# Kernel optimization log

Hardware: AMD Instinct MI355X
Metric: run time of the kernel (lower is better)

## Reference

```python
import jax, jax.numpy as jnp
import numpy as np

D_MODEL = 1024
NUM_HEADS = 16
HEAD_DIM = D_MODEL // NUM_HEADS
B, S = 4, 2048


def setup_inputs() -> dict:
    key = jax.random.key(0)
    ks = jax.random.split(key, 11)
    s = 1.0 / np.sqrt(D_MODEL)
    inp = {
        "query": jax.random.normal(ks[0], (B, S, D_MODEL), jnp.float32),
        "key": jax.random.normal(ks[1], (B, S, D_MODEL), jnp.float32),
        "value": jax.random.normal(ks[2], (B, S, D_MODEL), jnp.float32),
        "Wq": jax.random.uniform(ks[3], (D_MODEL, D_MODEL), jnp.float32, -s, s),
        "bq": jax.random.uniform(ks[4], (D_MODEL,), jnp.float32, -s, s),
        "Wk": jax.random.uniform(ks[5], (D_MODEL, D_MODEL), jnp.float32, -s, s),
        "bk": jax.random.uniform(ks[6], (D_MODEL,), jnp.float32, -s, s),
        "Wv": jax.random.uniform(ks[7], (D_MODEL, D_MODEL), jnp.float32, -s, s),
        "bv": jax.random.uniform(ks[8], (D_MODEL,), jnp.float32, -s, s),
        "Wo": jax.random.uniform(ks[9], (D_MODEL, D_MODEL), jnp.float32, -s, s),
        "bo": jax.random.uniform(ks[10], (D_MODEL,), jnp.float32, -s, s),
    }
    return inp


def reference(query, key, value, Wq, bq, Wk, bk, Wv, bv, Wo, bo):
    B_, Sq, _ = query.shape
    # torch Linear: x @ W.T + b
    q = (query @ Wq.T + bq).reshape(B_, Sq, NUM_HEADS, HEAD_DIM).transpose(0, 2, 1, 3)  # [B,H,Sq,Dh]
    k = (key @ Wk.T + bk).reshape(B_, -1, NUM_HEADS, HEAD_DIM).transpose(0, 2, 1, 3)
    v = (value @ Wv.T + bv).reshape(B_, -1, NUM_HEADS, HEAD_DIM).transpose(0, 2, 1, 3)
    scores = jnp.einsum("bhqd,bhkd->bhqk", q, k) / np.sqrt(HEAD_DIM)
    attn = jax.nn.softmax(scores, axis=-1)
    x = jnp.einsum("bhqk,bhkd->bhqd", attn, v)  # [B,H,Sq,Dh]
    x = x.transpose(0, 2, 1, 3).reshape(B_, Sq, D_MODEL)
    return x @ Wo.T + bo
```

## Files before the change

kernel.cpp:

```cpp
#include <hip/hip_runtime.h>
#include <hip/hip_bf16.h>
#include <stdint.h>


typedef __attribute__((ext_vector_type(4))) float f32x4;
typedef __attribute__((ext_vector_type(16))) float f32x16;
typedef __attribute__((ext_vector_type(8))) short short8;
typedef __attribute__((ext_vector_type(4))) unsigned short ushort4v;
typedef __attribute__((ext_vector_type(4))) unsigned int uint4v;

#define SCALE_Q 0.1803368801111f
#define EXP2(x) __builtin_amdgcn_exp2f(x)

__device__ __forceinline__ unsigned short f2bf(float f) {
    union { float f; unsigned int u; } v; v.f = f;
    unsigned int u = v.u;
    u += 0x7FFFu + ((u >> 16) & 1u);
    return (unsigned short)(u >> 16);
}

__device__ __forceinline__ void gll16(const void* g, void* l) {
    __builtin_amdgcn_global_load_lds(
        (const __attribute__((address_space(1))) void*)g,
        (__attribute__((address_space(3))) void*)l, 16, 0, 0);
}

__device__ __forceinline__ unsigned int cvtpk_bf16(float lo, float hi) {
    unsigned int r;
    asm("v_cvt_pk_bf16_f32 %0, %1, %2" : "=v"(r) : "v"(lo), "v"(hi));
    return r;
}
#define PLSWAP(a, b) asm("v_permlane32_swap_b32 %0, %1" : "+v"(a), "+v"(b))

__global__ __launch_bounds__(256) void cvtW(const float* __restrict__ s0, const float* __restrict__ s1,
                                            const float* __restrict__ s2, const float* __restrict__ s3,
                                            unsigned short* __restrict__ d0, unsigned short* __restrict__ d1,
                                            unsigned short* __restrict__ d2, unsigned short* __restrict__ d3) {
    int t = blockIdx.x >> 10;
    const float* sp = (t == 0) ? s0 : (t == 1) ? s1 : (t == 2) ? s2 : s3;
    unsigned short* dp = (t == 0) ? d0 : (t == 1) ? d1 : (t == 2) ? d2 : d3;
    int j = ((blockIdx.x & 1023) * 256 + threadIdx.x) * 4;
    float4 v = *(const float4*)(sp + j);
    ushort4v o; o.x = f2bf(v.x); o.y = f2bf(v.y); o.z = f2bf(v.z); o.w = f2bf(v.w);
    *(ushort4v*)(dp + j) = o;
}

__global__ __launch_bounds__(256, 2)
void proj3(const float* __restrict__ Aq, const float* __restrict__ Ak, const float* __restrict__ Av,
           const unsigned short* __restrict__ Wq, const unsigned short* __restrict__ Wk,
           const unsigned short* __restrict__ Wv,
           const float* __restrict__ bq, const float* __restrict__ bk, const float* __restrict__ bv,
           unsigned short* __restrict__ Cq, unsigned short* __restrict__ Ck,
           unsigned short* __restrict__ Cv) {
    __shared__ unsigned short As[128 * 32];
    __shared__ unsigned short Bs[128 * 32];
    const int tid = threadIdx.x;
    const int wid = tid >> 6, lane = tid & 63;
    const int seg = blockIdx.x >> 9, idx = blockIdx.x & 511;
    const float* Af = (seg == 0) ? Aq : (seg == 1) ? Ak : Av;
    const unsigned short* Bw = (seg == 0) ? Wq : (seg == 1) ? Wk : Wv;
    const float* bias = (seg == 0) ? bq : (seg == 1) ? bk : bv;
    unsigned short* C = (seg == 0) ? Cq : (seg == 1) ? Ck : Cv;

    const int xcd = idx & 7, j_ = idx >> 3;
    const int mtile = xcd * 8 + (j_ >> 3), ntile = j_ & 7;
    const int m0 = mtile * 128, n0 = ntile * 128;
    const int wm = (wid >> 1) * 64, wn = (wid & 1) * 64;

    f32x4 acc[4][4];
#pragma unroll
    for (int i = 0; i < 4; i++)
#pragma unroll
        for (int j = 0; j < 4; j++) acc[i][j] = f32x4{0.f, 0.f, 0.f, 0.f};

    const int srow = tid >> 2, scol = (tid & 3) * 8;
    const unsigned short* gB0 = Bw + (size_t)(n0 + srow) * 1024 + scol;
    const unsigned short* gB1 = Bw + (size_t)(n0 + 64 + srow) * 1024 + scol;
    char* lB0 = (char*)Bs + wid * 1024;
    char* lB1 = (char*)Bs + 4096 + wid * 1024;
    const float* gAf0 = Af + (size_t)(m0 + srow) * 1024 + scol;
    const float* gAf1 = Af + (size_t)(m0 + 64 + srow) * 1024 + scol;

    const int frow = lane & 15;
    const int fcol = (lane >> 4) * 16;

    float4 p00 = *(const float4*)(gAf0);
    float4 p01 = *(const float4*)(gAf0 + 4);
    float4 p10 = *(const float4*)(gAf1);
    float4 p11 = *(const float4*)(gAf1 + 4);

    for (int k0 = 0; k0 < 1024; k0 += 32) {
        gll16(gB0 + k0, lB0);
        gll16(gB1 + k0, lB1);
        {
            uint4v wa = {cvtpk_bf16(p00.x, p00.y), cvtpk_bf16(p00.z, p00.w),
                         cvtpk_bf16(p01.x, p01.y), cvtpk_bf16(p01.z, p01.w)};
            uint4v wb = {cvtpk_bf16(p10.x, p10.y), cvtpk_bf16(p10.z, p10.w),
                         cvtpk_bf16(p11.x, p11.y), cvtpk_bf16(p11.z, p11.w)};
            *(uint4v*)((char*)As + tid * 16) = wa;
            *(uint4v*)((char*)As + 4096 + tid * 16) = wb;
        }
        __syncthreads();
        if (k0 + 32 < 1024) {
            p00 = *(const float4*)(gAf0 + k0 + 32);
            p01 = *(const float4*)(gAf0 + k0 + 36);
            p10 = *(const float4*)(gAf1 + k0 + 32);
            p11 = *(const float4*)(gAf1 + k0 + 36);
        }
        short8 af[4], bfr[4];
#pragma unroll
        for (int i = 0; i < 4; i++)
            af[i] = *(const short8*)((const char*)As + (wm + i * 16 + frow) * 64 + fcol);
#pragma unroll
        for (int j = 0; j < 4; j++)
            bfr[j] = *(const short8*)((const char*)Bs + (wn + j * 16 + frow) * 64 + fcol);
#pragma unroll
        for (int i = 0; i < 4; i++)
#pragma unroll
            for (int j = 0; j < 4; j++)
                acc[i][j] = __builtin_amdgcn_mfma_f32_16x16x32_bf16(af[i], bfr[j], acc[i][j], 0, 0, 0);
        __syncthreads();
    }

    if (seg == 2) {
#pragma unroll
        for (int i = 0; i < 4; i++)
#pragma unroll
            for (int j = 0; j < 4; j++) {
                const int n = n0 + wn + j * 16 + (lane & 15);
                const float bv_ = bias[n];
                const int mbase = m0 + wm + i * 16 + (lane >> 4) * 4;
                ushort4v pk;
#pragma unroll
                for (int r = 0; r < 4; r++) pk[r] = f2bf(acc[i][j][r] + bv_);
                const int b = mbase >> 11, s = mbase & 2047;
                *(ushort4v*)(C + ((size_t)b * 1024 + n) * 2048 + s) = pk;
            }
    } else {
        const float scl = (seg == 0) ? SCALE_Q : 1.0f;
#pragma unroll
        for (int i = 0; i < 4; i++)
#pragma unroll
            for (int j = 0; j < 4; j++) {
                const int n = n0 + wn + j * 16 + (lane & 15);
                const float bv_ = bias[n];
#pragma unroll
                for (int r = 0; r < 4; r++) {
                    const int m = m0 + wm + i * 16 + (lane >> 4) * 4 + r;
                    C[(size_t)m * 1024 + n] = f2bf((acc[i][j][r] + bv_) * scl);
                }
            }
    }
}

__global__ __launch_bounds__(256, 2)
void gemm_out(const unsigned short* __restrict__ A, const unsigned short* __restrict__ Bw,
              const float* __restrict__ bias, float* __restrict__ C) {
    __shared__ unsigned short As[128 * 32];
    __shared__ unsigned short Bs[128 * 32];
    const int tid = threadIdx.x;
    const int wid = tid >> 6, lane = tid & 63;
    const int xcd = blockIdx.x & 7, j_ = blockIdx.x >> 3;
    const int mtile = xcd * 8 + (j_ >> 3), ntile = j_ & 7;
    const int m0 = mtile * 128, n0 = ntile * 128;
    const int wm = (wid >> 1) * 64, wn = (wid & 1) * 64;

    f32x4 acc[4][4];
#pragma unroll
    for (int i = 0; i < 4; i++)
#pragma unroll
        for (int j = 0; j < 4; j++) acc[i][j] = f32x4{0.f, 0.f, 0.f, 0.f};

    const int srow = tid >> 2, scol = (tid & 3) * 8;
    const unsigned short* gA0 = A + (size_t)(m0 + srow) * 1024 + scol;
    const unsigned short* gA1 = A + (size_t)(m0 + 64 + srow) * 1024 + scol;
    const unsigned short* gB0 = Bw + (size_t)(n0 + srow) * 1024 + scol;
    const unsigned short* gB1 = Bw + (size_t)(n0 + 64 + srow) * 1024 + scol;
    char* lA0 = (char*)As + wid * 1024;
    char* lA1 = (char*)As + 4096 + wid * 1024;
    char* lB0 = (char*)Bs + wid * 1024;
    char* lB1 = (char*)Bs + 4096 + wid * 1024;

    const int frow = lane & 15;
    const int fcol = (lane >> 4) * 16;

    for (int k0 = 0; k0 < 1024; k0 += 32) {
        gll16(gA0 + k0, lA0);
        gll16(gA1 + k0, lA1);
        gll16(gB0 + k0, lB0);
        gll16(gB1 + k0, lB1);
        __syncthreads();
        short8 af[4], bfr[4];
#pragma unroll
        for (int i = 0; i < 4; i++)
            af[i] = *(const short8*)((const char*)As + (wm + i * 16 + frow) * 64 + fcol);
#pragma unroll
        for (int j = 0; j < 4; j++)
            bfr[j] = *(const short8*)((const char*)Bs + (wn + j * 16 + frow) * 64 + fcol);
#pragma unroll
        for (int i = 0; i < 4; i++)
#pragma unroll
            for (int j = 0; j < 4; j++)
                acc[i][j] = __builtin_amdgcn_mfma_f32_16x16x32_bf16(af[i], bfr[j], acc[i][j], 0, 0, 0);
        __syncthreads();
    }

#pragma unroll
    for (int i = 0; i < 4; i++)
#pragma unroll
        for (int j = 0; j < 4; j++) {
            const int n = n0 + wn + j * 16 + (lane & 15);
            const float bv = bias[n];
#pragma unroll
            for (int r = 0; r < 4; r++) {
                const int m = m0 + wm + i * 16 + (lane >> 4) * 4 + r;
                C[(size_t)m * 1024 + n] = acc[i][j][r] + bv;
            }
        }
}

__global__ __launch_bounds__(256, 4)
void attn2(const unsigned short* __restrict__ Q, const unsigned short* __restrict__ K,
           const unsigned short* __restrict__ VT, unsigned short* __restrict__ O) {
    __shared__ unsigned short Kl[2][64 * 64];
    __shared__ unsigned short Vl[2][64 * 64];
    const int tid = threadIdx.x, wid = tid >> 6, lane = tid & 63;
    const int x = blockIdx.x;
    const int i_ = x >> 3;
    const int qt = i_ & 15;
    const int bh = (x & 7) + 8 * (i_ >> 4);
    const int b = bh >> 4, h = bh & 15;
    const int q0 = qt * 128 + wid * 32;
    const int qcol = lane & 31, g = lane >> 5;
    const int rx7 = qcol & 7;

    short8 bq[4];
    {
        const unsigned short* qp = Q + ((size_t)(b * 2048 + q0 + qcol)) * 1024 + h * 64 + g * 8;
#pragma unroll
        for (int ds = 0; ds < 4; ds++) bq[ds] = *(const short8*)(qp + ds * 16);
    }

    f32x16 oacc0, oacc1;
#pragma unroll
    for (int i = 0; i < 16; i++) { oacc0[i] = 0.f; oacc1[i] = 0.f; }
    float mrun = -1e30f, lrun = 0.f;

    const int srow = wid * 8 + (lane >> 3);
    const int sg = (lane & 7) ^ (lane >> 3);
    const unsigned short* gK0 = K + ((size_t)(b * 2048 + srow)) * 1024 + h * 64 + sg * 8;
    const unsigned short* gK1 = gK0 + (size_t)32 * 1024;
    const unsigned short* gV0 = VT + ((size_t)(b * 1024 + h * 64 + srow)) * 2048 + sg * 8;
    const unsigned short* gV1 = gV0 + (size_t)32 * 2048;

#define ATTN_STAGE(t_, bf_)                                                          \
    do {                                                                             \
        const size_t ko = (size_t)(t_) * 64 * 1024;                                  \
        const size_t vo = (size_t)(t_) * 64;                                         \
        gll16(gK0 + ko, (char*)Kl[bf_] + wid * 1024);                                \
        gll16(gK1 + ko, (char*)Kl[bf_] + 4096 + wid * 1024);                         \
        gll16(gV0 + vo, (char*)Vl[bf_] + wid * 1024);                                \
        gll16(gV1 + vo, (char*)Vl[bf_] + 4096 + wid * 1024);                         \
    } while (0)

    ATTN_STAGE(0, 0);

    for (int t = 0; t < 32; t++) {
        __syncthreads();
        if (t + 1 < 32) ATTN_STAGE(t + 1, (t + 1) & 1);
        const char* Kt = (const char*)Kl[t & 1];
        const char* Vt = (const char*)Vl[t & 1];

        f32x16 st0, st1;
#pragma unroll
        for (int i = 0; i < 16; i++) { st0[i] = 0.f; st1[i] = 0.f; }
        __builtin_amdgcn_s_setprio(1);
        {
            const char* kr0 = Kt + (qcol)*128;
            const char* kr1 = Kt + (32 + qcol) * 128;
#pragma unroll
            for (int ds = 0; ds < 4; ds++) {
                const int slot = ds * 2 + g;
                short8 a0 = *(const short8*)(kr0 + ((slot ^ rx7) << 4));
                short8 a1 = *(const short8*)(kr1 + ((slot ^ rx7) << 4));
                st0 = __builtin_amdgcn_mfma_f32_32x32x16_bf16(a0, bq[ds], st0, 0, 0, 0);
                st1 = __builtin_amdgcn_mfma_f32_32x32x16_bf16(a1, bq[ds], st1, 0, 0, 0);
            }
        }
        __builtin_amdgcn_s_setprio(0);

        float tm[8];
#pragma unroll
        for (int i = 0; i < 8; i++)
            tm[i] = fmaxf(fmaxf(st0[i], st0[i + 8]), fmaxf(st1[i], st1[i + 8]));
#pragma unroll
        for (int i = 0; i < 4; i++) tm[i] = fmaxf(tm[i], tm[i + 4]);
        float pm = fmaxf(fmaxf(tm[0], tm[1]), fmaxf(tm[2], tm[3]));
        pm = fmaxf(pm, __shfl_xor(pm, 32));

        if (!__all(pm <= mrun + 8.f)) {
            const float nm = fmaxf(mrun, pm);
            const float corr = EXP2(mrun - nm);
            mrun = nm;
            lrun *= corr;
#pragma unroll
            for (int i = 0; i < 16; i++) { oacc0[i] *= corr; oacc1[i] *= corr; }
        }

        f32x16 p0, p1;
#pragma unroll
        for (int i = 0; i < 16; i++) {
            p0[i] = EXP2(st0[i] - mrun);
            p1[i] = EXP2(st1[i] - mrun);
        }
        float ts[8];
#pragma unroll
        for (int i = 0; i < 8; i++) ts[i] = (p0[i] + p0[i + 8]) + (p1[i] + p1[i + 8]);
#pragma unroll
        for (int i = 0; i < 4; i++) ts[i] += ts[i + 4];
        float ps = (ts[0] + ts[1]) + (ts[2] + ts[3]);
        ps += __shfl_xor(ps, 32);
        lrun += ps;

        short8 pb[4];
        {
            unsigned int w[8];
#pragma unroll
            for (int p = 0; p < 8; p++) w[p] = cvtpk_bf16(p0[2 * p], p0[2 * p + 1]);
            PLSWAP(w[0], w[2]); PLSWAP(w[1], w[3]);
            PLSWAP(w[4], w[6]); PLSWAP(w[5], w[7]);
            uint4v lo = {w[0], w[1], w[2], w[3]};
            uint4v hi = {w[4], w[5], w[6], w[7]};
            pb[0] = __builtin_bit_cast(short8, lo);
            pb[1] = __builtin_bit_cast(short8, hi);
        }
        {
            unsigned int w[8];
#pragma unroll
            for (int p = 0; p < 8; p++) w[p] = cvtpk_bf16(p1[2 * p], p1[2 * p + 1]);
            PLSWAP(w[0], w[2]); PLSWAP(w[1], w[3]);
            PLSWAP(w[4], w[6]); PLSWAP(w[5], w[7]);
            uint4v lo = {w[0], w[1], w[2], w[3]};
            uint4v hi = {w[4], w[5], w[6], w[7]};
            pb[2] = __builtin_bit_cast(short8, lo);
            pb[3] = __builtin_bit_cast(short8, hi);
        }

        __builtin_amdgcn_s_setprio(1);
        {
            const char* vr0 = Vt + (qcol)*128;
            const char* vr1 = Vt + (32 + qcol) * 128;
#pragma unroll
            for (int kb = 0; kb < 4; kb++) {
                const int slot = kb * 2 + g;
                short8 a0 = *(const short8*)(vr0 + ((slot ^ rx7) << 4));
                short8 a1 = *(const short8*)(vr1 + ((slot ^ rx7) << 4));
                oacc0 = __builtin_amdgcn_mfma_f32_32x32x16_bf16(a0, pb[kb], oacc0, 0, 0, 0);
                oacc1 = __builtin_amdgcn_mfma_f32_32x32x16_bf16(a1, pb[kb], oacc1, 0, 0, 0);
            }
        }
        __builtin_amdgcn_s_setprio(0);
    }
#undef ATTN_STAGE

    const float inv = 1.f / lrun;
    unsigned short* orow = O + ((size_t)(b * 2048 + q0 + qcol)) * 1024 + h * 64;
#pragma unroll
    for (int dsub = 0; dsub < 2; dsub++)
#pragma unroll
        for (int q4 = 0; q4 < 4; q4++) {
            ushort4v pk;
#pragma unroll
            for (int rr = 0; rr < 4; rr++) {
                float v = (dsub == 0 ? oacc0[q4 * 4 + rr] : oacc1[q4 * 4 + rr]) * inv;
                pk[rr] = f2bf(v);
            }
            const int d0 = dsub * 32 + q4 * 8 + g * 4;
            *(ushort4v*)(orow + d0) = pk;
        }
}

extern "C" void kernel_launch(void* const* d_in, const int* in_sizes, int n_in,
                              void* d_out, int out_size, void* d_ws, size_t ws_size,
                              hipStream_t stream) {
    const float* query = (const float*)d_in[0];
    const float* key_  = (const float*)d_in[1];
    const float* value = (const float*)d_in[2];
    const float* Wq = (const float*)d_in[3];
    const float* bq = (const float*)d_in[4];
    const float* Wk = (const float*)d_in[5];
    const float* bk = (const float*)d_in[6];
    const float* Wv = (const float*)d_in[7];
    const float* bv = (const float*)d_in[8];
    const float* Wo = (const float*)d_in[9];
    const float* bo = (const float*)d_in[10];

    char* ws = (char*)d_ws;
    unsigned short* Xbf = (unsigned short*)(ws);
    unsigned short* Wqb = (unsigned short*)(ws + (16ull << 20));
    unsigned short* Wkb = (unsigned short*)(ws + (18ull << 20));
    unsigned short* Wvb = (unsigned short*)(ws + (20ull << 20));
    unsigned short* Wob = (unsigned short*)(ws + (22ull << 20));
    unsigned short* Qb  = (unsigned short*)(ws + (24ull << 20));
    unsigned short* Kb  = (unsigned short*)(ws + (40ull << 20));
    unsigned short* VTb = (unsigned short*)(ws + (56ull << 20));

    cvtW<<<4096, 256, 0, stream>>>(Wq, Wk, Wv, Wo, Wqb, Wkb, Wvb, Wob);

    proj3<<<1536, 256, 0, stream>>>(query, key_, value, Wqb, Wkb, Wvb,
                                    bq, bk, bv, Qb, Kb, VTb);

    attn2<<<1024, 256, 0, stream>>>(Qb, Kb, VTb, Xbf);

    gemm_out<<<512, 256, 0, stream>>>(Xbf, Wob, bo, (float*)d_out);
}
```

Before: 202.8 us.

## Double-buffer LDS tiles in projection and output GEMMs

```diff
diff --git a/kernel.cpp b/kernel.cpp
--- a/kernel.cpp
+++ b/kernel.cpp
@@ -52,8 +52,8 @@
            const float* __restrict__ bq, const float* __restrict__ bk, const float* __restrict__ bv,
            unsigned short* __restrict__ Cq, unsigned short* __restrict__ Ck,
            unsigned short* __restrict__ Cv) {
-    __shared__ unsigned short As[128 * 32];
-    __shared__ unsigned short Bs[128 * 32];
+    __shared__ unsigned short As[2][128 * 32];
+    __shared__ unsigned short Bs[2][128 * 32];
     const int tid = threadIdx.x;
     const int wid = tid >> 6, lane = tid & 63;
     const int seg = blockIdx.x >> 9, idx = blockIdx.x & 511;
@@ -76,8 +76,6 @@
     const int srow = tid >> 2, scol = (tid & 3) * 8;
     const unsigned short* gB0 = Bw + (size_t)(n0 + srow) * 1024 + scol;
     const unsigned short* gB1 = Bw + (size_t)(n0 + 64 + srow) * 1024 + scol;
-    char* lB0 = (char*)Bs + wid * 1024;
-    char* lB1 = (char*)Bs + 4096 + wid * 1024;
     const float* gAf0 = Af + (size_t)(m0 + srow) * 1024 + scol;
     const float* gAf1 = Af + (size_t)(m0 + 64 + srow) * 1024 + scol;
 
@@ -88,38 +86,55 @@
     float4 p01 = *(const float4*)(gAf0 + 4);
     float4 p10 = *(const float4*)(gAf1);
     float4 p11 = *(const float4*)(gAf1 + 4);
-
+    gll16(gB0, (char*)Bs[0] + wid * 1024);
+    gll16(gB1, (char*)Bs[0] + 4096 + wid * 1024);
+    {
+        uint4v wa = {cvtpk_bf16(p00.x, p00.y), cvtpk_bf16(p00.z, p00.w),
+                     cvtpk_bf16(p01.x, p01.y), cvtpk_bf16(p01.z, p01.w)};
+        uint4v wb = {cvtpk_bf16(p10.x, p10.y), cvtpk_bf16(p10.z, p10.w),
+                     cvtpk_bf16(p11.x, p11.y), cvtpk_bf16(p11.z, p11.w)};
+        *(uint4v*)((char*)As[0] + tid * 16) = wa;
+        *(uint4v*)((char*)As[0] + 4096 + tid * 16) = wb;
+    }
+    p00 = *(const float4*)(gAf0 + 32);
+    p01 = *(const float4*)(gAf0 + 36);
+    p10 = *(const float4*)(gAf1 + 32);
+    p11 = *(const float4*)(gAf1 + 36);
+    __syncthreads();
+
+    int c = 0;
     for (int k0 = 0; k0 < 1024; k0 += 32) {
-        gll16(gB0 + k0, lB0);
-        gll16(gB1 + k0, lB1);
-        {
+        const int kn = k0 + 32;
+        if (kn < 1024) {
+            gll16(gB0 + kn, (char*)Bs[c ^ 1] + wid * 1024);
+            gll16(gB1 + kn, (char*)Bs[c ^ 1] + 4096 + wid * 1024);
             uint4v wa = {cvtpk_bf16(p00.x, p00.y), cvtpk_bf16(p00.z, p00.w),
                          cvtpk_bf16(p01.x, p01.y), cvtpk_bf16(p01.z, p01.w)};
             uint4v wb = {cvtpk_bf16(p10.x, p10.y), cvtpk_bf16(p10.z, p10.w),
                          cvtpk_bf16(p11.x, p11.y), cvtpk_bf16(p11.z, p11.w)};
-            *(uint4v*)((char*)As + tid * 16) = wa;
-            *(uint4v*)((char*)As + 4096 + tid * 16) = wb;
-        }
-        __syncthreads();
-        if (k0 + 32 < 1024) {
-            p00 = *(const float4*)(gAf0 + k0 + 32);
-            p01 = *(const float4*)(gAf0 + k0 + 36);
-            p10 = *(const float4*)(gAf1 + k0 + 32);
-            p11 = *(const float4*)(gAf1 + k0 + 36);
+            *(uint4v*)((char*)As[c ^ 1] + tid * 16) = wa;
+            *(uint4v*)((char*)As[c ^ 1] + 4096 + tid * 16) = wb;
+            if (kn + 32 < 1024) {
+                p00 = *(const float4*)(gAf0 + kn + 32);
+                p01 = *(const float4*)(gAf0 + kn + 36);
+                p10 = *(const float4*)(gAf1 + kn + 32);
+                p11 = *(const float4*)(gAf1 + kn + 36);
+            }
         }
         short8 af[4], bfr[4];
 #pragma unroll
         for (int i = 0; i < 4; i++)
-            af[i] = *(const short8*)((const char*)As + (wm + i * 16 + frow) * 64 + fcol);
+            af[i] = *(const short8*)((const char*)As[c] + (wm + i * 16 + frow) * 64 + fcol);
 #pragma unroll
         for (int j = 0; j < 4; j++)
-            bfr[j] = *(const short8*)((const char*)Bs + (wn + j * 16 + frow) * 64 + fcol);
+            bfr[j] = *(const short8*)((const char*)Bs[c] + (wn + j * 16 + frow) * 64 + fcol);
 #pragma unroll
         for (int i = 0; i < 4; i++)
 #pragma unroll
             for (int j = 0; j < 4; j++)
                 acc[i][j] = __builtin_amdgcn_mfma_f32_16x16x32_bf16(af[i], bfr[j], acc[i][j], 0, 0, 0);
         __syncthreads();
+        c ^= 1;
     }
 
     if (seg == 2) {
@@ -156,8 +171,8 @@
 __global__ __launch_bounds__(256, 2)
 void gemm_out(const unsigned short* __restrict__ A, const unsigned short* __restrict__ Bw,
               const float* __restrict__ bias, float* __restrict__ C) {
-    __shared__ unsigned short As[128 * 32];
-    __shared__ unsigned short Bs[128 * 32];
+    __shared__ unsigned short As[2][128 * 32];
+    __shared__ unsigned short Bs[2][128 * 32];
     const int tid = threadIdx.x;
     const int wid = tid >> 6, lane = tid & 63;
     const int xcd = blockIdx.x & 7, j_ = blockIdx.x >> 3;
@@ -176,33 +191,39 @@
     const unsigned short* gA1 = A + (size_t)(m0 + 64 + srow) * 1024 + scol;
     const unsigned short* gB0 = Bw + (size_t)(n0 + srow) * 1024 + scol;
     const unsigned short* gB1 = Bw + (size_t)(n0 + 64 + srow) * 1024 + scol;
-    char* lA0 = (char*)As + wid * 1024;
-    char* lA1 = (char*)As + 4096 + wid * 1024;
-    char* lB0 = (char*)Bs + wid * 1024;
-    char* lB1 = (char*)Bs + 4096 + wid * 1024;
 
     const int frow = lane & 15;
     const int fcol = (lane >> 4) * 16;
 
+    gll16(gA0, (char*)As[0] + wid * 1024);
+    gll16(gA1, (char*)As[0] + 4096 + wid * 1024);
+    gll16(gB0, (char*)Bs[0] + wid * 1024);
+    gll16(gB1, (char*)Bs[0] + 4096 + wid * 1024);
+    __syncthreads();
+
+    int c = 0;
     for (int k0 = 0; k0 < 1024; k0 += 32) {
-        gll16(gA0 + k0, lA0);
-        gll16(gA1 + k0, lA1);
-        gll16(gB0 + k0, lB0);
-        gll16(gB1 + k0, lB1);
-        __syncthreads();
+        const int kn = k0 + 32;
+        if (kn < 1024) {
+            gll16(gA0 + kn, (char*)As[c ^ 1] + wid * 1024);
+            gll16(gA1 + kn, (char*)As[c ^ 1] + 4096 + wid * 1024);
+            gll16(gB0 + kn, (char*)Bs[c ^ 1] + wid * 1024);
+            gll16(gB1 + kn, (char*)Bs[c ^ 1] + 4096 + wid * 1024);
+        }
         short8 af[4], bfr[4];
 #pragma unroll
         for (int i = 0; i < 4; i++)
-            af[i] = *(const short8*)((const char*)As + (wm + i * 16 + frow) * 64 + fcol);
+            af[i] = *(const short8*)((const char*)As[c] + (wm + i * 16 + frow) * 64 + fcol);
 #pragma unroll
         for (int j = 0; j < 4; j++)
-            bfr[j] = *(const short8*)((const char*)Bs + (wn + j * 16 + frow) * 64 + fcol);
+            bfr[j] = *(const short8*)((const char*)Bs[c] + (wn + j * 16 + frow) * 64 + fcol);
 #pragma unroll
         for (int i = 0; i < 4; i++)
 #pragma unroll
             for (int j = 0; j < 4; j++)
                 acc[i][j] = __builtin_amdgcn_mfma_f32_16x16x32_bf16(af[i], bfr[j], acc[i][j], 0, 0, 0);
         __syncthreads();
+        c ^= 1;
     }
 
 #pragma unroll
```

Measured after the change: 201.9 us. About the same (-0.4%).

## Pre-convert activations to bf16 and use swizzled BK=64 direct-to-LDS GEMM tiles

Applied to the files above, without the earlier changes.

```diff
diff --git a/kernel.cpp b/kernel.cpp
--- a/kernel.cpp
+++ b/kernel.cpp
@@ -32,32 +32,49 @@
 }
 #define PLSWAP(a, b) asm("v_permlane32_swap_b32 %0, %1" : "+v"(a), "+v"(b))
 
-__global__ __launch_bounds__(256) void cvtW(const float* __restrict__ s0, const float* __restrict__ s1,
-                                            const float* __restrict__ s2, const float* __restrict__ s3,
-                                            unsigned short* __restrict__ d0, unsigned short* __restrict__ d1,
-                                            unsigned short* __restrict__ d2, unsigned short* __restrict__ d3) {
-    int t = blockIdx.x >> 10;
-    const float* sp = (t == 0) ? s0 : (t == 1) ? s1 : (t == 2) ? s2 : s3;
-    unsigned short* dp = (t == 0) ? d0 : (t == 1) ? d1 : (t == 2) ? d2 : d3;
-    int j = ((blockIdx.x & 1023) * 256 + threadIdx.x) * 4;
-    float4 v = *(const float4*)(sp + j);
-    ushort4v o; o.x = f2bf(v.x); o.y = f2bf(v.y); o.z = f2bf(v.z); o.w = f2bf(v.w);
-    *(ushort4v*)(dp + j) = o;
-}
-
-__global__ __launch_bounds__(256, 2)
-void proj3(const float* __restrict__ Aq, const float* __restrict__ Ak, const float* __restrict__ Av,
+__global__ __launch_bounds__(256) void cvtAll(
+    const float* __restrict__ q, const float* __restrict__ k, const float* __restrict__ v,
+    const float* __restrict__ wq, const float* __restrict__ wk,
+    const float* __restrict__ wv, const float* __restrict__ wo,
+    unsigned short* __restrict__ xq, unsigned short* __restrict__ xk, unsigned short* __restrict__ xv,
+    unsigned short* __restrict__ dwq, unsigned short* __restrict__ dwk,
+    unsigned short* __restrict__ dwv, unsigned short* __restrict__ dwo) {
+    const int bb = blockIdx.x;
+    const float* s;
+    unsigned short* d;
+    int jb;
+    if (bb < 4096) {
+        const int t = bb >> 10;
+        s = (t == 0) ? wq : (t == 1) ? wk : (t == 2) ? wv : wo;
+        d = (t == 0) ? dwq : (t == 1) ? dwk : (t == 2) ? dwv : dwo;
+        jb = bb & 1023;
+    } else {
+        const int r = bb - 4096;
+        const int a = r >> 13;
+        s = (a == 0) ? q : (a == 1) ? k : v;
+        d = (a == 0) ? xq : (a == 1) ? xk : xv;
+        jb = r & 8191;
+    }
+    const int j = (jb * 256 + threadIdx.x) * 4;
+    float4 vv = *(const float4*)(s + j);
+    ushort4v o; o.x = f2bf(vv.x); o.y = f2bf(vv.y); o.z = f2bf(vv.z); o.w = f2bf(vv.w);
+    *(ushort4v*)(d + j) = o;
+}
+
+__global__ __launch_bounds__(256, 3)
+void proj3(const unsigned short* __restrict__ Aq, const unsigned short* __restrict__ Ak,
+           const unsigned short* __restrict__ Av,
            const unsigned short* __restrict__ Wq, const unsigned short* __restrict__ Wk,
            const unsigned short* __restrict__ Wv,
            const float* __restrict__ bq, const float* __restrict__ bk, const float* __restrict__ bv,
            unsigned short* __restrict__ Cq, unsigned short* __restrict__ Ck,
            unsigned short* __restrict__ Cv) {
-    __shared__ unsigned short As[128 * 32];
-    __shared__ unsigned short Bs[128 * 32];
+    __shared__ unsigned short As[128 * 64];
+    __shared__ unsigned short Bs[128 * 64];
     const int tid = threadIdx.x;
     const int wid = tid >> 6, lane = tid & 63;
     const int seg = blockIdx.x >> 9, idx = blockIdx.x & 511;
-    const float* Af = (seg == 0) ? Aq : (seg == 1) ? Ak : Av;
+    const unsigned short* A = (seg == 0) ? Aq : (seg == 1) ? Ak : Av;
     const unsigned short* Bw = (seg == 0) ? Wq : (seg == 1) ? Wk : Wv;
     const float* bias = (seg == 0) ? bq : (seg == 1) ? bk : bv;
     unsigned short* C = (seg == 0) ? Cq : (seg == 1) ? Ck : Cv;
@@ -73,52 +90,40 @@
 #pragma unroll
         for (int j = 0; j < 4; j++) acc[i][j] = f32x4{0.f, 0.f, 0.f, 0.f};
 
-    const int srow = tid >> 2, scol = (tid & 3) * 8;
-    const unsigned short* gB0 = Bw + (size_t)(n0 + srow) * 1024 + scol;
-    const unsigned short* gB1 = Bw + (size_t)(n0 + 64 + srow) * 1024 + scol;
-    char* lB0 = (char*)Bs + wid * 1024;
-    char* lB1 = (char*)Bs + 4096 + wid * 1024;
-    const float* gAf0 = Af + (size_t)(m0 + srow) * 1024 + scol;
-    const float* gAf1 = Af + (size_t)(m0 + 64 + srow) * 1024 + scol;
+    const int sr8 = lane >> 3;
+    const int sg = (lane & 7) ^ sr8;
+    const unsigned short* gA = A + (size_t)(m0 + wid * 8 + sr8) * 1024 + sg * 8;
+    const unsigned short* gB = Bw + (size_t)(n0 + wid * 8 + sr8) * 1024 + sg * 8;
+    char* lA = (char*)As + wid * 1024;
+    char* lB = (char*)Bs + wid * 1024;
 
     const int frow = lane & 15;
-    const int fcol = (lane >> 4) * 16;
-
-    float4 p00 = *(const float4*)(gAf0);
-    float4 p01 = *(const float4*)(gAf0 + 4);
-    float4 p10 = *(const float4*)(gAf1);
-    float4 p11 = *(const float4*)(gAf1 + 4);
-
-    for (int k0 = 0; k0 < 1024; k0 += 32) {
-        gll16(gB0 + k0, lB0);
-        gll16(gB1 + k0, lB1);
-        {
-            uint4v wa = {cvtpk_bf16(p00.x, p00.y), cvtpk_bf16(p00.z, p00.w),
-                         cvtpk_bf16(p01.x, p01.y), cvtpk_bf16(p01.z, p01.w)};
-            uint4v wb = {cvtpk_bf16(p10.x, p10.y), cvtpk_bf16(p10.z, p10.w),
-                         cvtpk_bf16(p11.x, p11.y), cvtpk_bf16(p11.z, p11.w)};
-            *(uint4v*)((char*)As + tid * 16) = wa;
-            *(uint4v*)((char*)As + 4096 + tid * 16) = wb;
+    const int g4 = lane >> 4;
+    const int rx = lane & 7;
+
+    for (int k0 = 0; k0 < 1024; k0 += 64) {
+#pragma unroll
+        for (int r = 0; r < 4; r++) {
+            gll16(gA + k0 + r * 32 * 1024, lA + r * 4096);
+            gll16(gB + k0 + r * 32 * 1024, lB + r * 4096);
         }
         __syncthreads();
-        if (k0 + 32 < 1024) {
-            p00 = *(const float4*)(gAf0 + k0 + 32);
-            p01 = *(const float4*)(gAf0 + k0 + 36);
-            p10 = *(const float4*)(gAf1 + k0 + 32);
-            p11 = *(const float4*)(gAf1 + k0 + 36);
-        }
-        short8 af[4], bfr[4];
-#pragma unroll
-        for (int i = 0; i < 4; i++)
-            af[i] = *(const short8*)((const char*)As + (wm + i * 16 + frow) * 64 + fcol);
-#pragma unroll
-        for (int j = 0; j < 4; j++)
-            bfr[j] = *(const short8*)((const char*)Bs + (wn + j * 16 + frow) * 64 + fcol);
-#pragma unroll
-        for (int i = 0; i < 4; i++)
+#pragma unroll
+        for (int ks = 0; ks < 2; ks++) {
+            const int so = ((ks * 4 + g4) ^ rx) << 4;
+            short8 af[4], bfr[4];
+#pragma unroll
+            for (int i = 0; i < 4; i++)
+                af[i] = *(const short8*)((const char*)As + (wm + i * 16 + frow) * 128 + so);
 #pragma unroll
             for (int j = 0; j < 4; j++)
-                acc[i][j] = __builtin_amdgcn_mfma_f32_16x16x32_bf16(af[i], bfr[j], acc[i][j], 0, 0, 0);
+                bfr[j] = *(const short8*)((const char*)Bs + (wn + j * 16 + frow) * 128 + so);
+#pragma unroll
+            for (int i = 0; i < 4; i++)
+#pragma unroll
+                for (int j = 0; j < 4; j++)
+                    acc[i][j] = __builtin_amdgcn_mfma_f32_16x16x32_bf16(af[i], bfr[j], acc[i][j], 0, 0, 0);
+        }
         __syncthreads();
     }
 
@@ -153,11 +158,11 @@
     }
 }
 
-__global__ __launch_bounds__(256, 2)
+__global__ __launch_bounds__(256, 3)
 void gemm_out(const unsigned short* __restrict__ A, const unsigned short* __restrict__ Bw,
               const float* __restrict__ bias, float* __restrict__ C) {
-    __shared__ unsigned short As[128 * 32];
-    __shared__ unsigned short Bs[128 * 32];
+    __shared__ unsigned short As[128 * 64];
+    __shared__ unsigned short Bs[128 * 64];
     const int tid = threadIdx.x;
     const int wid = tid >> 6, lane = tid & 63;
     const int xcd = blockIdx.x & 7, j_ = blockIdx.x >> 3;
@@ -171,37 +176,40 @@
 #pragma unroll
         for (int j = 0; j < 4; j++) acc[i][j] = f32x4{0.f, 0.f, 0.f, 0.f};
 
-    const int srow = tid >> 2, scol = (tid & 3) * 8;
-    const unsigned short* gA0 = A + (size_t)(m0 + srow) * 1024 + scol;
-    const unsigned short* gA1 = A + (size_t)(m0 + 64 + srow) * 1024 + scol;
-    const unsigned short* gB0 = Bw + (size_t)(n0 + srow) * 1024 + scol;
-    const unsigned short* gB1 = Bw + (size_t)(n0 + 64 + srow) * 1024 + scol;
-    char* lA0 = (char*)As + wid * 1024;
-    char* lA1 = (char*)As + 4096 + wid * 1024;
-    char* lB0 = (char*)Bs + wid * 1024;
-    char* lB1 = (char*)Bs + 4096 + wid * 1024;
+    const int sr8 = lane >> 3;
+    const int sg = (lane & 7) ^ sr8;
+    const unsigned short* gA = A + (size_t)(m0 + wid * 8 + sr8) * 1024 + sg * 8;
+    const unsigned short* gB = Bw + (size_t)(n0 + wid * 8 + sr8) * 1024 + sg * 8;
+    char* lA = (char*)As + wid * 1024;
+    char* lB = (char*)Bs + wid * 1024;
 
     const int frow = lane & 15;
-    const int fcol = (lane >> 4) * 16;
-
-    for (int k0 = 0; k0 < 1024; k0 += 32) {
-        gll16(gA0 + k0, lA0);
-        gll16(gA1 + k0, lA1);
-        gll16(gB0 + k0, lB0);
-        gll16(gB1 + k0, lB1);
+    const int g4 = lane >> 4;
+    const int rx = lane & 7;
+
+    for (int k0 = 0; k0 < 1024; k0 += 64) {
+#pragma unroll
+        for (int r = 0; r < 4; r++) {
+            gll16(gA + k0 + r * 32 * 1024, lA + r * 4096);
+            gll16(gB + k0 + r * 32 * 1024, lB + r * 4096);
+        }
         __syncthreads();
-        short8 af[4], bfr[4];
-#pragma unroll
-        for (int i = 0; i < 4; i++)
-            af[i] = *(const short8*)((const char*)As + (wm + i * 16 + frow) * 64 + fcol);
-#pragma unroll
-        for (int j = 0; j < 4; j++)
-            bfr[j] = *(const short8*)((const char*)Bs + (wn + j * 16 + frow) * 64 + fcol);
-#pragma unroll
-        for (int i = 0; i < 4; i++)
+#pragma unroll
+        for (int ks = 0; ks < 2; ks++) {
+            const int so = ((ks * 4 + g4) ^ rx) << 4;
+            short8 af[4], bfr[4];
+#pragma unroll
+            for (int i = 0; i < 4; i++)
+                af[i] = *(const short8*)((const char*)As + (wm + i * 16 + frow) * 128 + so);
 #pragma unroll
             for (int j = 0; j < 4; j++)
-                acc[i][j] = __builtin_amdgcn_mfma_f32_16x16x32_bf16(af[i], bfr[j], acc[i][j], 0, 0, 0);
+                bfr[j] = *(const short8*)((const char*)Bs + (wn + j * 16 + frow) * 128 + so);
+#pragma unroll
+            for (int i = 0; i < 4; i++)
+#pragma unroll
+                for (int j = 0; j < 4; j++)
+                    acc[i][j] = __builtin_amdgcn_mfma_f32_16x16x32_bf16(af[i], bfr[j], acc[i][j], 0, 0, 0);
+        }
         __syncthreads();
     }
 
@@ -396,21 +404,24 @@
     const float* bo = (const float*)d_in[10];
 
     char* ws = (char*)d_ws;
-    unsigned short* Xbf = (unsigned short*)(ws);
-    unsigned short* Wqb = (unsigned short*)(ws + (16ull << 20));
-    unsigned short* Wkb = (unsigned short*)(ws + (18ull << 20));
-    unsigned short* Wvb = (unsigned short*)(ws + (20ull << 20));
-    unsigned short* Wob = (unsigned short*)(ws + (22ull << 20));
-    unsigned short* Qb  = (unsigned short*)(ws + (24ull << 20));
-    unsigned short* Kb  = (unsigned short*)(ws + (40ull << 20));
-    unsigned short* VTb = (unsigned short*)(ws + (56ull << 20));
-
-    cvtW<<<4096, 256, 0, stream>>>(Wq, Wk, Wv, Wo, Wqb, Wkb, Wvb, Wob);
-
-    proj3<<<1536, 256, 0, stream>>>(query, key_, value, Wqb, Wkb, Wvb,
+    unsigned short* Xq  = (unsigned short*)(ws);
+    unsigned short* Xk  = (unsigned short*)(ws + (16ull << 20));
+    unsigned short* Xv  = (unsigned short*)(ws + (32ull << 20));
+    unsigned short* Wqb = (unsigned short*)(ws + (48ull << 20));
+    unsigned short* Wkb = (unsigned short*)(ws + (50ull << 20));
+    unsigned short* Wvb = (unsigned short*)(ws + (52ull << 20));
+    unsigned short* Wob = (unsigned short*)(ws + (54ull << 20));
+    unsigned short* Qb  = (unsigned short*)(ws + (56ull << 20));
+    unsigned short* Kb  = (unsigned short*)(ws + (72ull << 20));
+    unsigned short* VTb = (unsigned short*)(ws + (88ull << 20));
+
+    cvtAll<<<28672, 256, 0, stream>>>(query, key_, value, Wq, Wk, Wv, Wo,
+                                      Xq, Xk, Xv, Wqb, Wkb, Wvb, Wob);
+
+    proj3<<<1536, 256, 0, stream>>>(Xq, Xk, Xv, Wqb, Wkb, Wvb,
                                     bq, bk, bv, Qb, Kb, VTb);
 
-    attn2<<<1024, 256, 0, stream>>>(Qb, Kb, VTb, Xbf);
-
-    gemm_out<<<512, 256, 0, stream>>>(Xbf, Wob, bo, (float*)d_out);
-}
+    attn2<<<1024, 256, 0, stream>>>(Qb, Kb, VTb, Xq);
+
+    gemm_out<<<512, 256, 0, stream>>>(Xq, Wob, bo, (float*)d_out);
+}
```

Measured after the change: 201.5 us. No clear change (-0.6%).
